# Performance work log

Measured on AMD Instinct MI355X. Metric: run time of the kernel, lower is better.

## Reference

```python
import jax, jax.numpy as jnp
import numpy as np

B = 64        # number of bags
D = 512       # feature dim
T = 131072    # total instances across all bags (ragged, avg ~2048/bag)


def setup_inputs() -> dict:
    key = jax.random.key(0)
    k_s, _ = jax.random.split(key)
    samples = jax.random.normal(k_s, (T, D), dtype=jnp.float32)
    # Ragged bag sizes that sum exactly to T (deterministic).
    rng = np.random.default_rng(0)
    w = rng.random(B)
    counts = np.floor(w / w.sum() * T).astype(np.int64)
    counts = np.maximum(counts, 1)
    counts[-1] += T - counts.sum()
    bags_num_samples = jnp.asarray(counts, dtype=jnp.int64)
    return {"samples": samples, "bags_num_samples": bags_num_samples}


def reference(samples, bags_num_samples):
    # Fused segmented mean-pool replacing the per-bag Python loop:
    # bag i owns rows [cum[i-1], cum[i]) of `samples`.
    n_bags = bags_num_samples.shape[0]
    total = samples.shape[0]
    seg_ids = jnp.repeat(jnp.arange(n_bags), bags_num_samples,
                         total_repeat_length=total)  # [T]
    sums = jax.ops.segment_sum(samples, seg_ids, num_segments=n_bags)  # [B, D]
    return sums / bags_num_samples[:, None].astype(samples.dtype)
```

## Files before the change

kernel.cpp:

```cpp
#include <hip/hip_runtime.h>

#define NBAGS 64
#define D 512
#define D4 128
#define NCHUNK 16

__global__ void agg_partial_kernel(const float* __restrict__ samples,
                                   const int* __restrict__ counts,
                                   float* __restrict__ partials) {
    const int bag   = blockIdx.x;
    const int chunk = blockIdx.y;

    long long off = 0, cnt = 0;
#pragma unroll
    for (int i = 0; i < NBAGS; ++i) {
        long long c = (long long)counts[i];
        off += (i < bag) ? c : 0;
        cnt  = (i == bag) ? c : cnt;
    }
    const long long r0 = off + (cnt * chunk) / NCHUNK;
    const long long r1 = off + (cnt * (chunk + 1)) / NCHUNK;

    const int t    = threadIdx.x;
    const int col  = t & (D4 - 1);
    const int half = t >> 7;

    const float4* __restrict__ src = (const float4*)samples;

    float4 acc = make_float4(0.f, 0.f, 0.f, 0.f);
    long long r = r0 + half;
    for (; r + 2 < r1; r += 4) {
        float4 v0 = src[r * D4 + col];
        float4 v1 = src[(r + 2) * D4 + col];
        acc.x += v0.x; acc.y += v0.y; acc.z += v0.z; acc.w += v0.w;
        acc.x += v1.x; acc.y += v1.y; acc.z += v1.z; acc.w += v1.w;
    }
    for (; r < r1; r += 2) {
        float4 v = src[r * D4 + col];
        acc.x += v.x; acc.y += v.y; acc.z += v.z; acc.w += v.w;
    }

    __shared__ float4 lds[D4];
    if (half == 1) lds[col] = acc;
    __syncthreads();
    if (half == 0) {
        float4 o = lds[col];
        acc.x += o.x; acc.y += o.y; acc.z += o.z; acc.w += o.w;
        ((float4*)partials)[(bag * NCHUNK + chunk) * D4 + col] = acc;
    }
}

__global__ void agg_reduce_kernel(const float* __restrict__ partials,
                                  const int* __restrict__ counts,
                                  float* __restrict__ out) {
    const int bag = blockIdx.x;
    const int col = threadIdx.x;

    const float4* __restrict__ p = (const float4*)partials;
    float4 acc = make_float4(0.f, 0.f, 0.f, 0.f);
#pragma unroll
    for (int c = 0; c < NCHUNK; ++c) {
        float4 v = p[(bag * NCHUNK + c) * D4 + col];
        acc.x += v.x; acc.y += v.y; acc.z += v.z; acc.w += v.w;
    }
    const float inv = 1.0f / (float)counts[bag];
    acc.x *= inv; acc.y *= inv; acc.z *= inv; acc.w *= inv;
    ((float4*)out)[bag * D4 + col] = acc;
}

extern "C" void kernel_launch(void* const* d_in, const int* in_sizes, int n_in,
                              void* d_out, int out_size, void* d_ws, size_t ws_size,
                              hipStream_t stream) {
    const float* samples  = (const float*)d_in[0];
    const int*   counts   = (const int*)d_in[1];
    float*       out      = (float*)d_out;
    float*       partials = (float*)d_ws;

    dim3 grid1(NBAGS, NCHUNK);
    agg_partial_kernel<<<grid1, 256, 0, stream>>>(samples, counts, partials);
    agg_reduce_kernel<<<NBAGS, D4, 0, stream>>>(partials, counts, out);
}
```

Before: 54.27 us.

## Split work into fixed-size row chunks instead of per-bag equal splits

Replaces the fixed 64x16 grid, where each bag is split into 16 equal chunks whose size depends on bag size, with a flat grid of 128-row chunks mapped to bags through a prefix scan over counts. This balances work across blocks regardless of ragged bag sizes and launches more blocks. The partial loop is also unrolled to four loads with two accumulators to raise memory-level parallelism. The cost is a data-dependent reduce loop, some idle blocks that exit early, and more partials to sum per bag.

```diff
diff --git a/kernel.cpp b/kernel.cpp
--- a/kernel.cpp
+++ b/kernel.cpp
@@ -3,23 +3,33 @@
 #define NBAGS 64
 #define D 512
 #define D4 128
-#define NCHUNK 16
+#define RPC 128
+#define TTOT 131072
+#define MAXCHUNKS (TTOT / RPC + NBAGS)
 
 __global__ void agg_partial_kernel(const float* __restrict__ samples,
                                    const int* __restrict__ counts,
                                    float* __restrict__ partials) {
-    const int bag   = blockIdx.x;
-    const int chunk = blockIdx.y;
+    const int g = blockIdx.x;
 
-    long long off = 0, cnt = 0;
+    int bag = -1, mychunk = 0;
+    long long rowbase = 0, cnt = 0;
+    {
+        long long cb = 0, rb = 0;
 #pragma unroll
-    for (int i = 0; i < NBAGS; ++i) {
-        long long c = (long long)counts[i];
-        off += (i < bag) ? c : 0;
-        cnt  = (i == bag) ? c : cnt;
+        for (int i = 0; i < NBAGS; ++i) {
+            long long c  = (long long)counts[i];
+            int       nc = (int)((c + RPC - 1) / RPC);
+            if (bag < 0 && g >= cb && g < cb + nc) {
+                bag = i; mychunk = (int)(g - cb); rowbase = rb; cnt = c;
+            }
+            cb += nc; rb += c;
+        }
     }
-    const long long r0 = off + (cnt * chunk) / NCHUNK;
-    const long long r1 = off + (cnt * (chunk + 1)) / NCHUNK;
+    if (bag < 0) return;
+
+    const long long r0 = rowbase + (long long)mychunk * RPC;
+    const long long r1 = min(rowbase + cnt, r0 + (long long)RPC);
 
     const int t    = threadIdx.x;
     const int col  = t & (D4 - 1);
@@ -27,26 +37,32 @@
 
     const float4* __restrict__ src = (const float4*)samples;
 
-    float4 acc = make_float4(0.f, 0.f, 0.f, 0.f);
+    float4 a0 = make_float4(0.f, 0.f, 0.f, 0.f);
+    float4 a1 = make_float4(0.f, 0.f, 0.f, 0.f);
     long long r = r0 + half;
-    for (; r + 2 < r1; r += 4) {
-        float4 v0 = src[r * D4 + col];
+    for (; r + 6 < r1; r += 8) {
+        float4 v0 = src[(r    ) * D4 + col];
         float4 v1 = src[(r + 2) * D4 + col];
-        acc.x += v0.x; acc.y += v0.y; acc.z += v0.z; acc.w += v0.w;
-        acc.x += v1.x; acc.y += v1.y; acc.z += v1.z; acc.w += v1.w;
+        float4 v2 = src[(r + 4) * D4 + col];
+        float4 v3 = src[(r + 6) * D4 + col];
+        a0.x += v0.x; a0.y += v0.y; a0.z += v0.z; a0.w += v0.w;
+        a1.x += v1.x; a1.y += v1.y; a1.z += v1.z; a1.w += v1.w;
+        a0.x += v2.x; a0.y += v2.y; a0.z += v2.z; a0.w += v2.w;
+        a1.x += v3.x; a1.y += v3.y; a1.z += v3.z; a1.w += v3.w;
     }
     for (; r < r1; r += 2) {
         float4 v = src[r * D4 + col];
-        acc.x += v.x; acc.y += v.y; acc.z += v.z; acc.w += v.w;
+        a0.x += v.x; a0.y += v.y; a0.z += v.z; a0.w += v.w;
     }
+    a0.x += a1.x; a0.y += a1.y; a0.z += a1.z; a0.w += a1.w;
 
     __shared__ float4 lds[D4];
-    if (half == 1) lds[col] = acc;
+    if (half == 1) lds[col] = a0;
     __syncthreads();
     if (half == 0) {
         float4 o = lds[col];
-        acc.x += o.x; acc.y += o.y; acc.z += o.z; acc.w += o.w;
-        ((float4*)partials)[(bag * NCHUNK + chunk) * D4 + col] = acc;
+        a0.x += o.x; a0.y += o.y; a0.z += o.z; a0.w += o.w;
+        ((float4*)partials)[(long long)g * D4 + col] = a0;
     }
 }
 
@@ -56,14 +72,22 @@
     const int bag = blockIdx.x;
     const int col = threadIdx.x;
 
+    long long cb = 0; int nc = 0; long long cnt = 0;
+#pragma unroll
+    for (int i = 0; i < NBAGS; ++i) {
+        long long c  = (long long)counts[i];
+        int       n  = (int)((c + RPC - 1) / RPC);
+        if (i == bag) { nc = n; cnt = c; break; }
+        cb += n;
+    }
+
     const float4* __restrict__ p = (const float4*)partials;
     float4 acc = make_float4(0.f, 0.f, 0.f, 0.f);
-#pragma unroll
-    for (int c = 0; c < NCHUNK; ++c) {
-        float4 v = p[(bag * NCHUNK + c) * D4 + col];
+    for (int c = 0; c < nc; ++c) {
+        float4 v = p[(cb + c) * D4 + col];
         acc.x += v.x; acc.y += v.y; acc.z += v.z; acc.w += v.w;
     }
-    const float inv = 1.0f / (float)counts[bag];
+    const float inv = 1.0f / (float)cnt;
     acc.x *= inv; acc.y *= inv; acc.z *= inv; acc.w *= inv;
     ((float4*)out)[bag * D4 + col] = acc;
 }
@@ -76,7 +100,6 @@
     float*       out      = (float*)d_out;
     float*       partials = (float*)d_ws;
 
-    dim3 grid1(NBAGS, NCHUNK);
-    agg_partial_kernel<<<grid1, 256, 0, stream>>>(samples, counts, partials);
+    agg_partial_kernel<<<MAXCHUNKS, 256, 0, stream>>>(samples, counts, partials);
     agg_reduce_kernel<<<NBAGS, D4, 0, stream>>>(partials, counts, out);
 }
```

Result: slower. 58.80 us (+8.3%).
